# Performance work log

Measured on AMD Instinct MI355X. Metric: run time of the kernel, lower is better.

Reference implementation:

```python
import jax, jax.numpy as jnp
from jax import lax
import numpy as np

B = 16
E, NH, FF, L = 768, 12, 3072, 8
D = E // NH  # 64, per-head dim
PATCH_DIM = 16 * 16 * 16  # 4096


def setup_inputs() -> dict:
    key = jax.random.key(0)
    ks = jax.random.split(key, 16)
    s = 0.02
    def n(k, shape):
        return jax.random.normal(k, shape, dtype=jnp.float32) * s
    return {
        "x": jax.random.normal(ks[0], (B, 512, 512, 3), dtype=jnp.float32),
        "conv1_w": n(ks[1], (3, 3, 3, 16)), "conv1_b": jnp.zeros((16,), jnp.float32),
        "conv2_w": n(ks[2], (3, 3, 16, 16)), "conv2_b": jnp.zeros((16,), jnp.float32),
        "proj_w": n(ks[3], (PATCH_DIM, E)), "proj_b": jnp.zeros((E,), jnp.float32),
        "Wq": n(ks[4], (L, E, E)), "bq": jnp.zeros((L, E), jnp.float32),
        "Wk": n(ks[5], (L, E, E)), "bk": jnp.zeros((L, E), jnp.float32),
        "Wv": n(ks[6], (L, E, E)), "bv": jnp.zeros((L, E), jnp.float32),
        "Wo": n(ks[7], (L, E, E)), "bo": jnp.zeros((L, E), jnp.float32),
        "W1": n(ks[8], (L, E, FF)), "b1": jnp.zeros((L, FF), jnp.float32),
        "W2": n(ks[9], (L, FF, E)), "b2": jnp.zeros((L, E), jnp.float32),
        "ln1_g": jnp.ones((L, E), jnp.float32), "ln1_b": jnp.zeros((L, E), jnp.float32),
        "ln2_g": jnp.ones((L, E), jnp.float32), "ln2_b": jnp.zeros((L, E), jnp.float32),
        "head_w": n(ks[10], (E, 1)), "head_b": jnp.zeros((1,), jnp.float32),
    }


def _ln(x, g, b, eps=1e-6):
    m = jnp.mean(x, axis=-1, keepdims=True)
    v = jnp.var(x, axis=-1, keepdims=True)
    return (x - m) * lax.rsqrt(v + eps) * g + b


def _forward(x, conv1_w, conv1_b, conv2_w, conv2_b, proj_w, proj_b,
             Wq, bq, Wk, bk, Wv, bv, Wo, bo, W1, b1, W2, b2,
             ln1_g, ln1_b, ln2_g, ln2_b, head_w, head_b):
    dn = ('NHWC', 'HWIO', 'NHWC')
    h = jax.nn.relu(lax.conv_general_dilated(x, conv1_w, (1, 1), 'VALID', dimension_numbers=dn) + conv1_b)
    h = lax.reduce_window(h, -jnp.inf, lax.max, (1, 2, 2, 1), (1, 2, 2, 1), 'VALID')  # (B,255,255,16)
    h = jax.nn.relu(lax.conv_general_dilated(h, conv2_w, (1, 1), 'VALID', dimension_numbers=dn) + conv2_b)
    h = lax.reduce_window(h, -jnp.inf, lax.max, (1, 2, 2, 1), (1, 2, 2, 1), 'VALID')  # (B,126,126,16)
    # tf.image.extract_patches 16x16 stride 16 SAME: pad 126 -> 128 (1 before, 1 after)
    h = jnp.pad(h, ((0, 0), (1, 1), (1, 1), (0, 0)))
    Bc = h.shape[0]
    patches = h.reshape(Bc, 8, 16, 8, 16, 16).transpose(0, 1, 3, 2, 4, 5).reshape(Bc, 64, PATCH_DIM)
    t = patches @ proj_w + proj_b  # (B,64,768)
    scale = 1.0 / jnp.sqrt(jnp.float32(D))  # tf code scales by sqrt(per-head key dim)
    for i in range(L):
        q = (t @ Wq[i] + bq[i]).reshape(Bc, -1, NH, D).transpose(0, 2, 1, 3)
        k = (t @ Wk[i] + bk[i]).reshape(Bc, -1, NH, D).transpose(0, 2, 1, 3)
        v = (t @ Wv[i] + bv[i]).reshape(Bc, -1, NH, D).transpose(0, 2, 1, 3)
        w = jax.nn.softmax(jnp.einsum('bhqd,bhkd->bhqk', q, k) * scale, axis=-1)
        a = jnp.einsum('bhqk,bhkd->bhqd', w, v)  # (B,H,S,D)
        # FAITHFUL to original: reshape (B,H,S,D) -> (B,S,E) directly (no transpose back)
        a = a.reshape(Bc, -1, E)
        a = a @ Wo[i] + bo[i]
        o1 = _ln(t + a, ln1_g[i], ln1_b[i])
        f = jax.nn.relu(o1 @ W1[i] + b1[i]) @ W2[i] + b2[i]
        t = _ln(o1 + f, ln2_g[i], ln2_b[i])
    pooled = jnp.mean(t, axis=1)  # GlobalAveragePooling1D
    return jax.nn.sigmoid(pooled @ head_w + head_b)


def reference(x, conv1_w, conv1_b, conv2_w, conv2_b, proj_w, proj_b,
              Wq, bq, Wk, bk, Wv, bv, Wo, bo, W1, b1, W2, b2,
              ln1_g, ln1_b, ln2_g, ln2_b, head_w, head_b):
    return _forward(x, conv1_w, conv1_b, conv2_w, conv2_b, proj_w, proj_b,
                    Wq, bq, Wk, bk, Wv, bv, Wo, bo, W1, b1, W2, b2,
                    ln1_g, ln1_b, ln2_g, ln2_b, head_w, head_b)
```

## Files before the change

kernel.cpp:

```cpp
#include <hip/hip_runtime.h>
#include <hip/hip_bf16.h>
#include <cstdint>
#include <cstddef>

typedef __bf16 bf16;
typedef __attribute__((ext_vector_type(8))) __bf16 bf16x8;
typedef __attribute__((ext_vector_type(4))) float f32x4;

__global__ __launch_bounds__(256) void wtrans(const float* __restrict__ src,
    bf16* __restrict__ dst, int K, int N) {
  __shared__ float tile[32][33];
  int l = blockIdx.z;
  src += (size_t)l * K * N; dst += (size_t)l * K * N;
  int n0 = blockIdx.x * 32, k0 = blockIdx.y * 32;
  int tx = threadIdx.x & 31, ty = threadIdx.x >> 5;
#pragma unroll
  for (int i = 0; i < 4; i++) {
    int k = ty + i * 8;
    tile[k][tx] = src[(size_t)(k0 + k) * N + n0 + tx];
  }
  __syncthreads();
#pragma unroll
  for (int i = 0; i < 4; i++) {
    int n = ty + i * 8;
    dst[(size_t)(n0 + n) * K + k0 + tx] = (bf16)tile[tx][n];
  }
}

__global__ __launch_bounds__(256) void conv1_pool(const float* __restrict__ x,
    const float* __restrict__ w, const float* __restrict__ bias,
    bf16* __restrict__ out) {
  __shared__ float ws[432];
  __shared__ float bs[16];
  int t = threadIdx.x;
  for (int i = t; i < 432; i += 256) ws[i] = w[i];
  if (t < 16) bs[t] = bias[t];
  __syncthreads();
  int idx = blockIdx.x * 256 + t;
  if (idx >= 16 * 255 * 255) return;
  int xo = idx % 255; int tmp = idx / 255; int yo = tmp % 255; int b = tmp / 255;
  float best[16];
#pragma unroll
  for (int c = 0; c < 16; c++) best[c] = 0.f;
#pragma unroll
  for (int py = 0; py < 2; py++)
#pragma unroll
  for (int px = 0; px < 2; px++) {
    float acc[16];
#pragma unroll
    for (int c = 0; c < 16; c++) acc[c] = bs[c];
    int iy0 = yo * 2 + py, ix0 = xo * 2 + px;
    for (int ky = 0; ky < 3; ky++)
    for (int kx = 0; kx < 3; kx++) {
      const float* xp = x + ((size_t)(b * 512 + iy0 + ky) * 512 + (ix0 + kx)) * 3;
      float v0 = xp[0], v1 = xp[1], v2 = xp[2];
      const float* wp = &ws[((ky * 3 + kx) * 3) * 16];
#pragma unroll
      for (int c = 0; c < 16; c++) acc[c] = fmaf(v0, wp[c], acc[c]);
#pragma unroll
      for (int c = 0; c < 16; c++) acc[c] = fmaf(v1, wp[16 + c], acc[c]);
#pragma unroll
      for (int c = 0; c < 16; c++) acc[c] = fmaf(v2, wp[32 + c], acc[c]);
    }
#pragma unroll
    for (int c = 0; c < 16; c++) best[c] = fmaxf(best[c], acc[c]);
  }
  bf16* op = out + (size_t)idx * 16;
#pragma unroll
  for (int c = 0; c < 16; c++) op[c] = (bf16)best[c];
}

#define C2STR 20
__global__ __launch_bounds__(256) void conv2_pool_patch(const bf16* __restrict__ in,
    const float* __restrict__ w, const float* __restrict__ bias,
    bf16* __restrict__ patches) {
  __shared__ bf16 xs[34 * 34 * C2STR];
  __shared__ float ws[2304];
  __shared__ float bs[16];
  int t = threadIdx.x;
  int tx = blockIdx.x, ty = blockIdx.y, b = blockIdx.z;
  for (int i = t; i < 2304; i += 256) ws[i] = w[i];
  if (t < 16) bs[t] = bias[t];
  int r0 = 32 * ty - 2, c0 = 32 * tx - 2;
  for (int i = t; i < 1156; i += 256) {
    int rr = i / 34, cc = i % 34;
    int gr = min(max(r0 + rr, 0), 254), gc = min(max(c0 + cc, 0), 254);
    const bf16* ip = in + ((size_t)(b * 255 + gr) * 255 + gc) * 16;
    uint4 v0 = *(const uint4*)ip;
    uint4 v1 = *(const uint4*)(ip + 8);
    bf16* op = &xs[i * C2STR];
    *(uint4*)op = v0;
    *(uint4*)(op + 8) = v1;
  }
  __syncthreads();
  int py_ = t >> 4, px_ = t & 15;
  int yp = ty * 16 + py_, xp = tx * 16 + px_;
  bf16* op = patches + ((size_t)(b * 64 + ty * 8 + tx) * 4096 + py_ * 256 + px_ * 16);
  if (yp == 0 || yp == 127 || xp == 0 || xp == 127) {
#pragma unroll
    for (int c = 0; c < 16; c++) op[c] = (bf16)0.f;
    return;
  }
  float best[16];
#pragma unroll
  for (int c = 0; c < 16; c++) best[c] = 0.f;
  for (int py = 0; py < 2; py++)
  for (int px = 0; px < 2; px++) {
    float acc[16];
#pragma unroll
    for (int c = 0; c < 16; c++) acc[c] = bs[c];
    for (int ky = 0; ky < 3; ky++)
    for (int kx = 0; kx < 3; kx++) {
      int lr_ = 2 * py_ + py + ky, lc_ = 2 * px_ + px + kx;
      const bf16* xpp = &xs[(lr_ * 34 + lc_) * C2STR];
      const float* wp = &ws[(ky * 3 + kx) * 256];
#pragma unroll
      for (int ci = 0; ci < 16; ci++) {
        float v = (float)xpp[ci];
#pragma unroll
        for (int c = 0; c < 16; c++) acc[c] = fmaf(v, wp[ci * 16 + c], acc[c]);
      }
    }
#pragma unroll
    for (int c = 0; c < 16; c++) best[c] = fmaxf(best[c], acc[c]);
  }
#pragma unroll
  for (int c = 0; c < 16; c++) op[c] = (bf16)best[c];
}

#define LSTR 72

template<int MODE>
__device__ __forceinline__ void gemm_core(const bf16* __restrict__ A,
    const bf16* __restrict__ Bt, const float* __restrict__ bias,
    float* __restrict__ Cf, bf16* __restrict__ Cb,
    int bm, int bn, int N, int K, int k0, int kc) {
  __shared__ alignas(16) bf16 As[64 * LSTR];
  __shared__ alignas(16) bf16 Bs[64 * LSTR];
  int t = threadIdx.x, lane = t & 63, wave = t >> 6;
  int wm = (wave >> 1) * 32, wn = (wave & 1) * 32;
  int lq = lane >> 4, lr = lane & 15;
  f32x4 acc[2][2];
#pragma unroll
  for (int i = 0; i < 2; i++)
#pragma unroll
  for (int j = 0; j < 2; j++) acc[i][j] = (f32x4){0.f, 0.f, 0.f, 0.f};
  int r = t >> 2, c = (t & 3) * 16;
  const bf16* Ap = A + (size_t)(bm + r) * K + k0 + c;
  const bf16* Bp = Bt + (size_t)(bn + r) * K + k0 + c;
  bf16* AsW = &As[r * LSTR + c];
  bf16* BsW = &Bs[r * LSTR + c];
  uint4 a0 = *(const uint4*)Ap, a1 = *(const uint4*)(Ap + 8);
  uint4 b0 = *(const uint4*)Bp, b1 = *(const uint4*)(Bp + 8);
  for (int kk = 64; kk <= kc; kk += 64) {
    *(uint4*)AsW = a0; *(uint4*)(AsW + 8) = a1;
    *(uint4*)BsW = b0; *(uint4*)(BsW + 8) = b1;
    __syncthreads();
    if (kk < kc) {
      Ap += 64; Bp += 64;
      a0 = *(const uint4*)Ap; a1 = *(const uint4*)(Ap + 8);
      b0 = *(const uint4*)Bp; b1 = *(const uint4*)(Bp + 8);
    }
#pragma unroll
    for (int ks = 0; ks < 2; ks++) {
      bf16x8 af0 = *(const bf16x8*)&As[(wm + lr) * LSTR + ks * 32 + lq * 8];
      bf16x8 af1 = *(const bf16x8*)&As[(wm + 16 + lr) * LSTR + ks * 32 + lq * 8];
      bf16x8 bfr0 = *(const bf16x8*)&Bs[(wn + lr) * LSTR + ks * 32 + lq * 8];
      bf16x8 bfr1 = *(const bf16x8*)&Bs[(wn + 16 + lr) * LSTR + ks * 32 + lq * 8];
      acc[0][0] = __builtin_amdgcn_mfma_f32_16x16x32_bf16(af0, bfr0, acc[0][0], 0, 0, 0);
      acc[0][1] = __builtin_amdgcn_mfma_f32_16x16x32_bf16(af0, bfr1, acc[0][1], 0, 0, 0);
      acc[1][0] = __builtin_amdgcn_mfma_f32_16x16x32_bf16(af1, bfr0, acc[1][0], 0, 0, 0);
      acc[1][1] = __builtin_amdgcn_mfma_f32_16x16x32_bf16(af1, bfr1, acc[1][1], 0, 0, 0);
    }
    __syncthreads();
  }
#pragma unroll
  for (int mi = 0; mi < 2; mi++)
#pragma unroll
  for (int ni = 0; ni < 2; ni++) {
    int col = bn + wn + ni * 16 + lr;
#pragma unroll
    for (int rr = 0; rr < 4; rr++) {
      int row = bm + wm + mi * 16 + lq * 4 + rr;
      float v = acc[mi][ni][rr];
      if (MODE == 1) {
        v = fmaxf(v + bias[col], 0.f);
        Cb[(size_t)row * N + col] = (bf16)v;
      } else {
        Cf[(size_t)row * N + col] = v;
      }
    }
  }
}

template<int MODE>
__global__ __launch_bounds__(256) void gemm_std(const bf16* __restrict__ A,
    const bf16* __restrict__ Bt, const float* __restrict__ bias,
    float* __restrict__ Cf, bf16* __restrict__ Cb, int N, int K, int KC) {
  int s = blockIdx.z;
  float* Cfp = Cf ? Cf + (size_t)s * 1024 * N : nullptr;
  gemm_core<MODE>(A, Bt, bias, Cfp, Cb, blockIdx.y * 64, blockIdx.x * 64, N, K, s * KC, KC);
}

__global__ __launch_bounds__(256) void gemm_qkv(const bf16* __restrict__ A,
    const bf16* __restrict__ Btq, const bf16* __restrict__ Btk, const bf16* __restrict__ Btv,
    float* __restrict__ qp, float* __restrict__ kp, float* __restrict__ vp) {
  int z = blockIdx.z;
  int sel = z >> 1, s = z & 1;
  const bf16* Bt = (sel == 0) ? Btq : (sel == 1) ? Btk : Btv;
  float* C = ((sel == 0) ? qp : (sel == 1) ? kp : vp) + (size_t)s * 786432;
  gemm_core<0>(A, Bt, nullptr, C, nullptr, blockIdx.y * 64, blockIdx.x * 64, 768, 768, s * 384, 384);
}

__global__ __launch_bounds__(256) void attn_kernel(const float* __restrict__ Qp,
    const float* __restrict__ Kp, const float* __restrict__ Vp,
    const float* __restrict__ bq, const float* __restrict__ bk, const float* __restrict__ bv,
    bf16* __restrict__ Aout) {
  __shared__ alignas(16) float qs[64 * 68];
  __shared__ alignas(16) float ks[64 * 68];
  __shared__ alignas(16) float ss[64 * 68];
  int t = threadIdx.x;
  int bh = blockIdx.x; int b = bh / 12, h = bh % 12;
  size_t base = (size_t)b * 49152 + h * 64;
  const float* qb0 = Qp + base; const float* qb1 = qb0 + 786432;
  const float* kb0 = Kp + base; const float* kb1 = kb0 + 786432;
  const float* vb0 = Vp + base; const float* vb1 = vb0 + 786432;
  {
    int s = t >> 2, qd = (t & 3) * 16;
#pragma unroll
    for (int j = 0; j < 16; j += 4) {
      float4 q0 = *(const float4*)(qb0 + (size_t)s * 768 + qd + j);
      float4 q1 = *(const float4*)(qb1 + (size_t)s * 768 + qd + j);
      float4 qb4 = *(const float4*)(bq + h * 64 + qd + j);
      float4 k0 = *(const float4*)(kb0 + (size_t)s * 768 + qd + j);
      float4 k1 = *(const float4*)(kb1 + (size_t)s * 768 + qd + j);
      float4 kb4 = *(const float4*)(bk + h * 64 + qd + j);
      qs[s * 68 + qd + j + 0] = q0.x + q1.x + qb4.x;
      qs[s * 68 + qd + j + 1] = q0.y + q1.y + qb4.y;
      qs[s * 68 + qd + j + 2] = q0.z + q1.z + qb4.z;
      qs[s * 68 + qd + j + 3] = q0.w + q1.w + qb4.w;
      ks[s * 68 + qd + j + 0] = k0.x + k1.x + kb4.x;
      ks[s * 68 + qd + j + 1] = k0.y + k1.y + kb4.y;
      ks[s * 68 + qd + j + 2] = k0.z + k1.z + kb4.z;
      ks[s * 68 + qd + j + 3] = k0.w + k1.w + kb4.w;
    }
  }
  __syncthreads();
  int r = t >> 4, c = t & 15;
  {
    float sc[4][4];
#pragma unroll
    for (int i = 0; i < 4; i++)
#pragma unroll
    for (int j = 0; j < 4; j++) sc[i][j] = 0.f;
    for (int k = 0; k < 64; k += 4) {
      float4 qv[4], kv[4];
#pragma unroll
      for (int i = 0; i < 4; i++) qv[i] = *(const float4*)&qs[(r + 16 * i) * 68 + k];
#pragma unroll
      for (int j = 0; j < 4; j++) kv[j] = *(const float4*)&ks[(c + 16 * j) * 68 + k];
#pragma unroll
      for (int i = 0; i < 4; i++)
#pragma unroll
      for (int j = 0; j < 4; j++)
        sc[i][j] += qv[i].x * kv[j].x + qv[i].y * kv[j].y + qv[i].z * kv[j].z + qv[i].w * kv[j].w;
    }
#pragma unroll
    for (int i = 0; i < 4; i++)
#pragma unroll
    for (int j = 0; j < 4; j++)
      ss[(r + 16 * i) * 68 + c + 16 * j] = sc[i][j] * 0.125f;
  }
  __syncthreads();
  {
    int d = t & 63, s0 = (t >> 6) * 16;
    float bvd = bv[h * 64 + d];
    alignas(16) float vv[16];
#pragma unroll
    for (int i = 0; i < 16; i++)
      vv[i] = vb0[(size_t)(s0 + i) * 768 + d] + vb1[(size_t)(s0 + i) * 768 + d] + bvd;
#pragma unroll
    for (int i = 0; i < 16; i += 4) *(float4*)&qs[d * 68 + s0 + i] = *(float4*)&vv[i];
  }
  {
    int lane = t & 63, wave = t >> 6;
    for (int rr = 0; rr < 16; rr++) {
      int row = wave * 16 + rr;
      float v = ss[row * 68 + lane];
      float m = v;
#pragma unroll
      for (int off = 32; off > 0; off >>= 1) m = fmaxf(m, __shfl_xor(m, off));
      float e = __expf(v - m);
      float ssum = e;
#pragma unroll
      for (int off = 32; off > 0; off >>= 1) ssum += __shfl_xor(ssum, off);
      ss[row * 68 + lane] = e / ssum;
    }
  }
  __syncthreads();
  {
    float oc[4][4];
#pragma unroll
    for (int i = 0; i < 4; i++)
#pragma unroll
    for (int j = 0; j < 4; j++) oc[i][j] = 0.f;
    for (int k = 0; k < 64; k += 4) {
      float4 pv[4], vv[4];
#pragma unroll
      for (int i = 0; i < 4; i++) pv[i] = *(const float4*)&ss[(r + 16 * i) * 68 + k];
#pragma unroll
      for (int j = 0; j < 4; j++) vv[j] = *(const float4*)&qs[(c + 16 * j) * 68 + k];
#pragma unroll
      for (int i = 0; i < 4; i++)
#pragma unroll
      for (int j = 0; j < 4; j++)
        oc[i][j] += pv[i].x * vv[j].x + pv[i].y * vv[j].y + pv[i].z * vv[j].z + pv[i].w * vv[j].w;
    }
    bf16* ob = Aout + (size_t)b * 49152 + h * 4096;
#pragma unroll
    for (int i = 0; i < 4; i++)
#pragma unroll
    for (int j = 0; j < 4; j++)
      ob[(r + 16 * i) * 64 + c + 16 * j] = (bf16)oc[i][j];
  }
}

template<int S>
__global__ __launch_bounds__(256) void ln_kernel(const float* __restrict__ X,
    const float* __restrict__ Y, const float* __restrict__ yb,
    const float* __restrict__ g, const float* __restrict__ bta,
    float* __restrict__ Of, bf16* __restrict__ Ob) {
  int row = blockIdx.x, t = threadIdx.x;
  const float* xp = X + (size_t)row * 768;
  float vals[3]; float s = 0.f, s2 = 0.f;
#pragma unroll
  for (int i = 0; i < 3; i++) {
    int e = t + 256 * i;
    float v = xp[e] + yb[e];
#pragma unroll
    for (int p = 0; p < S; p++) v += Y[(size_t)p * 786432 + (size_t)row * 768 + e];
    vals[i] = v; s += v; s2 = fmaf(v, v, s2);
  }
#pragma unroll
  for (int off = 32; off > 0; off >>= 1) { s += __shfl_xor(s, off); s2 += __shfl_xor(s2, off); }
  __shared__ float rs[4], rs2[4];
  if ((t & 63) == 0) { rs[t >> 6] = s; rs2[t >> 6] = s2; }
  __syncthreads();
  s = rs[0] + rs[1] + rs[2] + rs[3];
  s2 = rs2[0] + rs2[1] + rs2[2] + rs2[3];
  float mean = s * (1.f / 768.f);
  float var = s2 * (1.f / 768.f) - mean * mean;
  float rstd = rsqrtf(var + 1e-6f);
  float* ofp = Of + (size_t)row * 768;
  bf16* obp = Ob + (size_t)row * 768;
#pragma unroll
  for (int i = 0; i < 3; i++) {
    int e = t + 256 * i;
    float o = (vals[i] - mean) * rstd * g[e] + bta[e];
    ofp[e] = o; obp[e] = (bf16)o;
  }
}

__global__ __launch_bounds__(256) void reduce2(const float* __restrict__ P,
    const float* __restrict__ bias, float* __restrict__ Of, bf16* __restrict__ Ob) {
  int row = blockIdx.x, t = threadIdx.x;
#pragma unroll
  for (int i = 0; i < 3; i++) {
    int e = t + 256 * i;
    float v = P[(size_t)row * 768 + e] + P[786432 + (size_t)row * 768 + e] + bias[e];
    Of[(size_t)row * 768 + e] = v;
    Ob[(size_t)row * 768 + e] = (bf16)v;
  }
}

__global__ __launch_bounds__(256) void head_kernel(const float* __restrict__ T,
    const float* __restrict__ hw, const float* __restrict__ hbp, float* __restrict__ out) {
  int b = blockIdx.x, t = threadIdx.x;
  float acc = 0.f;
#pragma unroll
  for (int i = 0; i < 3; i++) {
    int e = t + 256 * i;
    float s = 0.f;
    for (int si = 0; si < 64; si++) s += T[(size_t)(b * 64 + si) * 768 + e];
    acc = fmaf(s * (1.f / 64.f), hw[e], acc);
  }
#pragma unroll
  for (int off = 32; off > 0; off >>= 1) acc += __shfl_xor(acc, off);
  __shared__ float rs[4];
  if ((t & 63) == 0) rs[t >> 6] = acc;
  __syncthreads();
  if (t == 0) {
    float z = rs[0] + rs[1] + rs[2] + rs[3] + hbp[0];
    out[b] = 1.f / (1.f + expf(-z));
  }
}

extern "C" void kernel_launch(void* const* d_in, const int* in_sizes, int n_in,
                              void* d_out, int out_size, void* d_ws, size_t ws_size,
                              hipStream_t stream) {
  const float* x     = (const float*)d_in[0];
  const float* c1w   = (const float*)d_in[1];
  const float* c1b   = (const float*)d_in[2];
  const float* c2w   = (const float*)d_in[3];
  const float* c2b   = (const float*)d_in[4];
  const float* projw = (const float*)d_in[5];
  const float* projb = (const float*)d_in[6];
  const float* Wq    = (const float*)d_in[7];
  const float* bq    = (const float*)d_in[8];
  const float* Wk    = (const float*)d_in[9];
  const float* bk    = (const float*)d_in[10];
  const float* Wv    = (const float*)d_in[11];
  const float* bv    = (const float*)d_in[12];
  const float* Wo    = (const float*)d_in[13];
  const float* bo    = (const float*)d_in[14];
  const float* W1    = (const float*)d_in[15];
  const float* b1    = (const float*)d_in[16];
  const float* W2    = (const float*)d_in[17];
  const float* b2    = (const float*)d_in[18];
  const float* ln1g  = (const float*)d_in[19];
  const float* ln1b  = (const float*)d_in[20];
  const float* ln2g  = (const float*)d_in[21];
  const float* ln2b  = (const float*)d_in[22];
  const float* headw = (const float*)d_in[23];
  const float* headb = (const float*)d_in[24];
  float* out = (float*)d_out;

  char* wp = (char*)d_ws;
  auto alloc = [&](size_t bytes) { char* p = wp; wp += (bytes + 255) & ~(size_t)255; return p; };
  bf16* c1p     = (bf16*)alloc((size_t)16 * 255 * 255 * 16 * 2);
  bf16* patches = (bf16*)alloc((size_t)1024 * 4096 * 2);
  bf16* projT   = (bf16*)alloc((size_t)4096 * 768 * 2);
  bf16* WqT     = (bf16*)alloc((size_t)8 * 768 * 768 * 2);
  bf16* WkT     = (bf16*)alloc((size_t)8 * 768 * 768 * 2);
  bf16* WvT     = (bf16*)alloc((size_t)8 * 768 * 768 * 2);
  bf16* WoT     = (bf16*)alloc((size_t)8 * 768 * 768 * 2);
  bf16* W1T     = (bf16*)alloc((size_t)8 * 768 * 3072 * 2);
  bf16* W2T     = (bf16*)alloc((size_t)8 * 3072 * 768 * 2);
  float* pp     = (float*)alloc((size_t)2 * 1024 * 768 * 4);
  float* tf     = (float*)alloc((size_t)1024 * 768 * 4);
  bf16*  tb     = (bf16*)alloc((size_t)1024 * 768 * 2);
  float* qp     = (float*)alloc((size_t)2 * 1024 * 768 * 4);
  float* kp     = (float*)alloc((size_t)2 * 1024 * 768 * 4);
  float* vp     = (float*)alloc((size_t)2 * 1024 * 768 * 4);
  float* wop    = (float*)alloc((size_t)2 * 1024 * 768 * 4);
  float* w2p    = (float*)alloc((size_t)4 * 1024 * 768 * 4);
  bf16*  ab     = (bf16*)alloc((size_t)1024 * 768 * 2);
  float* o1f    = (float*)alloc((size_t)1024 * 768 * 4);
  bf16*  o1b    = (bf16*)alloc((size_t)1024 * 768 * 2);
  bf16*  hbuf   = (bf16*)alloc((size_t)1024 * 3072 * 2);

  wtrans<<<dim3(24, 128, 1), 256, 0, stream>>>(projw, projT, 4096, 768);
  wtrans<<<dim3(24, 24, 8), 256, 0, stream>>>(Wq, WqT, 768, 768);
  wtrans<<<dim3(24, 24, 8), 256, 0, stream>>>(Wk, WkT, 768, 768);
  wtrans<<<dim3(24, 24, 8), 256, 0, stream>>>(Wv, WvT, 768, 768);
  wtrans<<<dim3(24, 24, 8), 256, 0, stream>>>(Wo, WoT, 768, 768);
  wtrans<<<dim3(96, 24, 8), 256, 0, stream>>>(W1, W1T, 768, 3072);
  wtrans<<<dim3(24, 96, 8), 256, 0, stream>>>(W2, W2T, 3072, 768);

  conv1_pool<<<4065, 256, 0, stream>>>(x, c1w, c1b, c1p);
  conv2_pool_patch<<<dim3(8, 8, 16), 256, 0, stream>>>(c1p, c2w, c2b, patches);
  gemm_std<0><<<dim3(12, 16, 2), 256, 0, stream>>>(patches, projT, nullptr, pp, nullptr, 768, 4096, 2048);
  reduce2<<<1024, 256, 0, stream>>>(pp, projb, tf, tb);

  for (int i = 0; i < 8; i++) {
    gemm_qkv<<<dim3(12, 16, 6), 256, 0, stream>>>(tb,
        WqT + (size_t)i * 589824, WkT + (size_t)i * 589824, WvT + (size_t)i * 589824,
        qp, kp, vp);
    attn_kernel<<<192, 256, 0, stream>>>(qp, kp, vp,
        bq + i * 768, bk + i * 768, bv + i * 768, ab);
    gemm_std<0><<<dim3(12, 16, 2), 256, 0, stream>>>(ab, WoT + (size_t)i * 589824,
        nullptr, wop, nullptr, 768, 768, 384);
    ln_kernel<2><<<1024, 256, 0, stream>>>(tf, wop, bo + i * 768,
        ln1g + i * 768, ln1b + i * 768, o1f, o1b);
    gemm_std<1><<<dim3(48, 16, 1), 256, 0, stream>>>(o1b, W1T + (size_t)i * 2359296,
        b1 + i * 3072, nullptr, hbuf, 3072, 768, 768);
    gemm_std<0><<<dim3(12, 16, 4), 256, 0, stream>>>(hbuf, W2T + (size_t)i * 2359296,
        nullptr, w2p, nullptr, 768, 3072, 768);
    ln_kernel<4><<<1024, 256, 0, stream>>>(o1f, w2p, b2 + i * 768,
        ln2g + i * 768, ln2b + i * 768, tf, tb);
  }
  head_kernel<<<16, 256, 0, stream>>>(tf, headw, headb, out);
}
```

Measured before the change: 1.128 ms.

## Compute conv2 with bf16 MFMA as implicit GEMM over taps and channels

Rewrites the second convolution+pool+patch kernel so each wave runs an implicit GEMM with 16x16x32 bf16 MFMA instructions. The kernel packs 9 taps x 16 input channels into 5 K-chunks, padding the last chunk with zeros, and splits the input tile into low and high channel planes in shared memory. It then does the 2x2 max pool across accumulator lanes and adds bias and ReLU afterwards. This targets the heavy scalar FMA loop in the old kernel. The trade-off is that conv weights are now rounded to bf16, and some of the padded K work is wasted.

```diff
diff --git a/kernel.cpp b/kernel.cpp
--- a/kernel.cpp
+++ b/kernel.cpp
@@ -70,62 +70,76 @@
   for (int c = 0; c < 16; c++) op[c] = (bf16)best[c];
 }
 
-#define C2STR 20
-__global__ __launch_bounds__(256) void conv2_pool_patch(const bf16* __restrict__ in,
+__global__ __launch_bounds__(256) void conv2_mfma(const bf16* __restrict__ in,
     const float* __restrict__ w, const float* __restrict__ bias,
     bf16* __restrict__ patches) {
-  __shared__ bf16 xs[34 * 34 * C2STR];
+  __shared__ alignas(16) bf16 xlo[1156 * 8];
+  __shared__ alignas(16) bf16 xhi[1156 * 8];
   __shared__ float ws[2304];
-  __shared__ float bs[16];
   int t = threadIdx.x;
   int tx = blockIdx.x, ty = blockIdx.y, b = blockIdx.z;
   for (int i = t; i < 2304; i += 256) ws[i] = w[i];
-  if (t < 16) bs[t] = bias[t];
   int r0 = 32 * ty - 2, c0 = 32 * tx - 2;
   for (int i = t; i < 1156; i += 256) {
     int rr = i / 34, cc = i % 34;
     int gr = min(max(r0 + rr, 0), 254), gc = min(max(c0 + cc, 0), 254);
     const bf16* ip = in + ((size_t)(b * 255 + gr) * 255 + gc) * 16;
-    uint4 v0 = *(const uint4*)ip;
-    uint4 v1 = *(const uint4*)(ip + 8);
-    bf16* op = &xs[i * C2STR];
-    *(uint4*)op = v0;
-    *(uint4*)(op + 8) = v1;
-  }
-  __syncthreads();
-  int py_ = t >> 4, px_ = t & 15;
-  int yp = ty * 16 + py_, xp = tx * 16 + px_;
-  bf16* op = patches + ((size_t)(b * 64 + ty * 8 + tx) * 4096 + py_ * 256 + px_ * 16);
-  if (yp == 0 || yp == 127 || xp == 0 || xp == 127) {
-#pragma unroll
-    for (int c = 0; c < 16; c++) op[c] = (bf16)0.f;
-    return;
-  }
-  float best[16];
-#pragma unroll
-  for (int c = 0; c < 16; c++) best[c] = 0.f;
-  for (int py = 0; py < 2; py++)
-  for (int px = 0; px < 2; px++) {
-    float acc[16];
-#pragma unroll
-    for (int c = 0; c < 16; c++) acc[c] = bs[c];
-    for (int ky = 0; ky < 3; ky++)
-    for (int kx = 0; kx < 3; kx++) {
-      int lr_ = 2 * py_ + py + ky, lc_ = 2 * px_ + px + kx;
-      const bf16* xpp = &xs[(lr_ * 34 + lc_) * C2STR];
-      const float* wp = &ws[(ky * 3 + kx) * 256];
-#pragma unroll
-      for (int ci = 0; ci < 16; ci++) {
-        float v = (float)xpp[ci];
-#pragma unroll
-        for (int c = 0; c < 16; c++) acc[c] = fmaf(v, wp[ci * 16 + c], acc[c]);
+    *(uint4*)&xlo[i * 8] = *(const uint4*)ip;
+    *(uint4*)&xhi[i * 8] = *(const uint4*)(ip + 8);
+  }
+  __syncthreads();
+  int lane = t & 63, wave = t >> 6;
+  int lr = lane & 15, lq = lane >> 4;
+  int tapsel = lq >> 1;
+  int ci0 = (lq & 1) * 8;
+  bf16x8 bfrag[5];
+  int koff[5];
+#pragma unroll
+  for (int c2 = 0; c2 < 5; c2++) {
+    int tap = 2 * c2 + tapsel;
+    bf16x8 v;
+#pragma unroll
+    for (int j = 0; j < 8; j++)
+      v[j] = (tap < 9) ? (bf16)ws[tap * 256 + (ci0 + j) * 16 + lr] : (bf16)0.f;
+    bfrag[c2] = v;
+    int tc = min(tap, 8);
+    koff[c2] = (tc / 3) * 34 + (tc % 3);
+  }
+  const bf16* plane = (lq & 1) ? xhi : xlo;
+  float bco = bias[lr];
+  bf16* pout = patches + ((size_t)(b * 64 + ty * 8 + tx) * 4096);
+#pragma unroll
+  for (int yy = 0; yy < 4; yy++) {
+    int Y = wave * 4 + yy;
+    int yp = ty * 16 + Y;
+    bool padrow = (yp == 0 || yp == 127);
+#pragma unroll
+    for (int hx = 0; hx < 2; hx++) {
+      f32x4 a0 = {0.f, 0.f, 0.f, 0.f}, a1 = {0.f, 0.f, 0.f, 0.f};
+      int base0 = (2 * Y) * 34 + hx * 16 + lr;
+      int base1 = base0 + 34;
+#pragma unroll
+      for (int c2 = 0; c2 < 5; c2++) {
+        bf16x8 f0 = *(const bf16x8*)&plane[(base0 + koff[c2]) * 8];
+        a0 = __builtin_amdgcn_mfma_f32_16x16x32_bf16(f0, bfrag[c2], a0, 0, 0, 0);
       }
-    }
-#pragma unroll
-    for (int c = 0; c < 16; c++) best[c] = fmaxf(best[c], acc[c]);
-  }
-#pragma unroll
-  for (int c = 0; c < 16; c++) op[c] = (bf16)best[c];
+#pragma unroll
+      for (int c2 = 0; c2 < 5; c2++) {
+        bf16x8 f1 = *(const bf16x8*)&plane[(base1 + koff[c2]) * 8];
+        a1 = __builtin_amdgcn_mfma_f32_16x16x32_bf16(f1, bfrag[c2], a1, 0, 0, 0);
+      }
+      float m0 = fmaxf(fmaxf(a0[0], a0[1]), fmaxf(a1[0], a1[1]));
+      float m1 = fmaxf(fmaxf(a0[2], a0[3]), fmaxf(a1[2], a1[3]));
+      m0 = fmaxf(m0 + bco, 0.f);
+      m1 = fmaxf(m1 + bco, 0.f);
+      int px0 = hx * 8 + 2 * lq, px1 = px0 + 1;
+      int xp0 = tx * 16 + px0, xp1 = xp0 + 1;
+      if (padrow || xp0 == 0) m0 = 0.f;
+      if (padrow || xp1 == 127) m1 = 0.f;
+      pout[Y * 256 + px0 * 16 + lr] = (bf16)m0;
+      pout[Y * 256 + px1 * 16 + lr] = (bf16)m1;
+    }
+  }
 }
 
 #define LSTR 72
@@ -458,7 +472,7 @@
   wtrans<<<dim3(24, 96, 8), 256, 0, stream>>>(W2, W2T, 3072, 768);
 
   conv1_pool<<<4065, 256, 0, stream>>>(x, c1w, c1b, c1p);
-  conv2_pool_patch<<<dim3(8, 8, 16), 256, 0, stream>>>(c1p, c2w, c2b, patches);
+  conv2_mfma<<<dim3(8, 8, 16), 256, 0, stream>>>(c1p, c2w, c2b, patches);
   gemm_std<0><<<dim3(12, 16, 2), 256, 0, stream>>>(patches, projT, nullptr, pp, nullptr, 768, 4096, 2048);
   reduce2<<<1024, 256, 0, stream>>>(pp, projb, tf, tb);
 
```

After: 1.055 ms. 1.07x faster.
